# Performance work log

Measured on AMD Instinct MI355X. Metric: run time of the kernel, lower is better.

The kernel has to match this reference:

```python
import jax, jax.numpy as jnp
import numpy as np

IOU_THRESH = 0.5
NEG_POS_RATIO = 3
VAR0, VAR1 = 0.1, 0.2  # BoxCoder variances


def box_iou(a, b):
    # a: [G,4] xyxy, b: [P,4] xyxy -> [G,P]
    lt = jnp.maximum(a[:, None, :2], b[None, :, :2])
    rb = jnp.minimum(a[:, None, 2:], b[None, :, 2:])
    wh = jnp.clip(rb - lt, 0.0)
    inter = wh[..., 0] * wh[..., 1]
    area_a = (a[:, 2] - a[:, 0]) * (a[:, 3] - a[:, 1])
    area_b = (b[:, 2] - b[:, 0]) * (b[:, 3] - b[:, 1])
    return inter / (area_a[:, None] + area_b[None, :] - inter)


def xywha_to_xyxy(p):
    c, wh = p[:, :2], p[:, 2:]
    return jnp.concatenate([c - wh * 0.5, c + wh * 0.5], axis=-1)


def assign_targets(gt_boxes, gt_labels, priors_xyxy):
    # gt_boxes [G,4], gt_labels [G], priors_xyxy [P,4]
    iou = box_iou(gt_boxes, priors_xyxy)            # [G,P]
    matched_vals = iou.max(axis=0)                  # [P]
    matches = iou.argmax(axis=0)                    # [P]
    best_prior = iou.argmax(axis=1)                 # [G] best prior per target
    G = gt_boxes.shape[0]
    matches = matches.at[best_prior].set(jnp.arange(G))
    matched_vals = matched_vals.at[best_prior].set(2.0)
    labels = jnp.where(matched_vals < IOU_THRESH, 0, gt_labels[matches])  # [P]
    boxes = gt_boxes[matches]                       # [P,4]
    return boxes, labels


def encode(boxes_xyxy, priors_xywha):
    # SSD center-form encoding with variances
    ctr = (boxes_xyxy[:, :2] + boxes_xyxy[:, 2:]) * 0.5
    wh = boxes_xyxy[:, 2:] - boxes_xyxy[:, :2]
    g_c = (ctr - priors_xywha[:, :2]) / (VAR0 * priors_xywha[:, 2:])
    g_wh = jnp.log(wh / priors_xywha[:, 2:]) / VAR1
    return jnp.concatenate([g_c, g_wh], axis=-1)


def hard_negative_mask(bg_loss, labels):
    # bg_loss [B,P]: -log_softmax(logits)[...,0]; keep all positives and
    # top-(ratio*num_pos) hardest negatives per image.
    pos = labels > 0
    num_neg = pos.sum(axis=1, keepdims=True) * NEG_POS_RATIO
    loss = jnp.where(pos, -jnp.inf, bg_loss)
    order = jnp.argsort(-loss, axis=1)
    rank = jnp.argsort(order, axis=1)
    return pos | (rank < num_neg)


def reference(priors, class_logits, box_regression, gt_boxes, gt_labels):
    priors_xyxy = xywha_to_xyxy(priors)
    boxes, labels = jax.vmap(assign_targets, in_axes=(0, 0, None))(
        gt_boxes, gt_labels, priors_xyxy)            # [B,P,4], [B,P]
    regression_targets = jax.vmap(encode, in_axes=(0, None))(boxes, priors)

    logp = jax.nn.log_softmax(class_logits, axis=-1)  # [B,P,C]
    bg_loss = jax.lax.stop_gradient(-logp[..., 0])
    mask = hard_negative_mask(bg_loss, labels)        # [B,P] bool

    # masked cross-entropy, reduction='sum'
    ce = -jnp.take_along_axis(logp, labels[..., None], axis=-1)[..., 0]
    loss_classifier = jnp.sum(jnp.where(mask, ce, 0.0))

    # masked smooth-L1 (beta=1), reduction='sum' over positives
    pos = labels > 0
    d = jnp.abs(box_regression - regression_targets)
    sl1 = jnp.where(d < 1.0, 0.5 * d * d, d - 0.5)
    loss_box_reg = jnp.sum(jnp.where(pos[..., None], sl1, 0.0))

    num_pos = jnp.sum(pos).astype(class_logits.dtype)
    return loss_box_reg / num_pos, loss_classifier / num_pos


def setup_inputs() -> dict:
    key = jax.random.key(0)
    ks = jax.random.split(key, 8)
    B, P, C, G = 64, 8732, 81, 16
    # priors: xywha in [0,1] with small positive wh
    p_c = jax.random.uniform(ks[0], (P, 2), jnp.float32, 0.05, 0.95)
    p_wh = jax.random.uniform(ks[1], (P, 2), jnp.float32, 0.02, 0.25)
    priors = jnp.concatenate([p_c, p_wh], axis=-1)
    class_logits = jax.random.normal(ks[2], (B, P, C), jnp.float32)
    box_regression = jax.random.normal(ks[3], (B, P, 4), jnp.float32)
    # gt boxes: valid xyxy in [0,1] with positive size
    g_c = jax.random.uniform(ks[4], (B, G, 2), jnp.float32, 0.2, 0.8)
    g_wh = jax.random.uniform(ks[5], (B, G, 2), jnp.float32, 0.05, 0.3)
    gt_boxes = jnp.concatenate([g_c - g_wh * 0.5, g_c + g_wh * 0.5], axis=-1)
    gt_labels = jax.random.randint(ks[6], (B, G), 1, C, jnp.int32)
    return {"priors": priors, "class_logits": class_logits,
            "box_regression": box_regression, "gt_boxes": gt_boxes,
            "gt_labels": gt_labels}
```

## Files before the change

### kernel.cpp

```cpp
#include <hip/hip_runtime.h>
#include <cfloat>

#define GT 16
#define NCLS 81
#define TPB 256
#define BPT 1024
#define MAXP 8732
#define TROWS 64
#define WF4 324
#define TF4 (TROWS*NCLS/4)

__device__ __forceinline__ float smoothl1(float d){
  float a = fabsf(d);
  return a < 1.0f ? 0.5f*a*a : a - 0.5f;
}

__global__ __launch_bounds__(BPT) void bestprior(
    const float* __restrict__ priors,
    const float* __restrict__ gt_boxes,
    int*   __restrict__ best,
    float* __restrict__ ce_pos, float* __restrict__ sl1_sum,
    int* __restrict__ num_pos, float* __restrict__ out, int P)
{
  const int b = blockIdx.x;
  const int tid = threadIdx.x, wave = tid >> 6, lane = tid & 63;
  __shared__ float gx0[GT], gy0[GT], gx1[GT], gy1[GT], ga[GT];
  __shared__ float redv[16*GT]; __shared__ int redi[16*GT];
  if (tid == 0){ ce_pos[b] = 0.0f; sl1_sum[b] = 0.0f; num_pos[b] = 0; }
  if (b == 0 && tid < 2) out[tid] = 0.0f;
  if (tid < GT){
    const float4 gb = ((const float4*)gt_boxes)[b*GT + tid];
    gx0[tid]=gb.x; gy0[tid]=gb.y; gx1[tid]=gb.z; gy1[tid]=gb.w;
    ga[tid] = (gb.z-gb.x)*(gb.w-gb.y);
  }
  __syncthreads();
  float bv[GT]; int bi[GT];
  #pragma unroll
  for (int g=0; g<GT; ++g){ bv[g] = -1.0f; bi[g] = 0x7fffffff; }
  for (int p = tid; p < P; p += BPT){
    const float4 pr = ((const float4*)priors)[p];
    const float px0 = pr.x - pr.z*0.5f, py0 = pr.y - pr.w*0.5f;
    const float px1 = pr.x + pr.z*0.5f, py1 = pr.y + pr.w*0.5f;
    const float pa = (px1-px0)*(py1-py0);
    #pragma unroll
    for (int g=0; g<GT; ++g){
      const float w = fmaxf(fminf(gx1[g],px1) - fmaxf(gx0[g],px0), 0.0f);
      const float h = fmaxf(fminf(gy1[g],py1) - fmaxf(gy0[g],py0), 0.0f);
      const float inter = w*h;
      const float iou = inter / (ga[g] + pa - inter);
      if (iou > bv[g]){ bv[g] = iou; bi[g] = p; }
    }
  }
  #pragma unroll
  for (int g=0; g<GT; ++g){
    float v = bv[g]; int i = bi[g];
    for (int off=32; off>0; off>>=1){
      const float ov = __shfl_down(v, off);
      const int   oi = __shfl_down(i, off);
      if (ov > v || (ov == v && oi < i)){ v = ov; i = oi; }
    }
    if (lane == 0){ redv[wave*GT+g] = v; redi[wave*GT+g] = i; }
  }
  __syncthreads();
  if (tid < GT){
    float v = redv[tid]; int i = redi[tid];
    for (int w=1; w<16; ++w){
      const float ov = redv[w*GT+tid]; const int oi = redi[w*GT+tid];
      if (ov > v || (ov == v && oi < i)){ v = ov; i = oi; }
    }
    best[b*GT + tid] = i;
  }
}

__global__ __launch_bounds__(TPB) void fused_lse(
    const float* __restrict__ priors,
    const float* __restrict__ gt_boxes,
    const int*   __restrict__ gt_labels,
    const float* __restrict__ box_reg,
    const int*   __restrict__ best,
    const float* __restrict__ logits,
    float* __restrict__ bg,
    float* __restrict__ ce_pos,
    float* __restrict__ sl1_sum,
    int*   __restrict__ num_pos,
    int P, int NT)
{
  __shared__ float s[TROWS*NCLS];
  const int tid = threadIdx.x;
  const int wave = tid >> 6, lane = tid & 63;
  const int rl = lane >> 2, q = lane & 3;
  const int c0 = q ? (1+20*q) : 0;
  const int c1 = 21 + 20*q;
  const int G = gridDim.x;
  int t = blockIdx.x;
  if (t >= NT) return;

  float4 r0,r1,r2,r3,r4,r5;
  {
    const float4* src = (const float4*)logits + (long long)t*TF4 + wave*WF4;
    r0 = src[lane]; r1 = src[lane+64]; r2 = src[lane+128];
    r3 = src[lane+192]; r4 = src[lane+256];
    if (lane < 4) r5 = src[lane+320];
  }
  float4* sd = (float4*)(s) + wave*WF4;
  const float* x = s + wave*(WF4*4) + rl*NCLS;
  for (; t < NT; t += G){
    sd[lane] = r0; sd[lane+64] = r1; sd[lane+128] = r2;
    sd[lane+192] = r3; sd[lane+256] = r4;
    if (lane < 4) sd[lane+320] = r5;
    const int tn = t + G;
    if (tn < NT){
      const float4* src = (const float4*)logits + (long long)tn*TF4 + wave*WF4;
      r0 = src[lane]; r1 = src[lane+64]; r2 = src[lane+128];
      r3 = src[lane+192]; r4 = src[lane+256];
      if (lane < 4) r5 = src[lane+320];
    }

    const int row = t*TROWS + wave*16 + rl;
    const int b = row / P;
    const int p = row - b*P;
    int lab = 0;
    if (q == 0){
      const float4 pr = ((const float4*)priors)[p];
      const float px0 = pr.x - pr.z*0.5f, py0 = pr.y - pr.w*0.5f;
      const float px1 = pr.x + pr.z*0.5f, py1 = pr.y + pr.w*0.5f;
      const float pa = (px1-px0)*(py1-py0);
      const float4* gtb4 = (const float4*)gt_boxes + b*GT;
      float mv = -1.0f; int mi = 0;
      #pragma unroll
      for (int g=0; g<GT; ++g){
        const float4 gb = gtb4[g];
        const float w = fmaxf(fminf(gb.z,px1) - fmaxf(gb.x,px0), 0.0f);
        const float h = fmaxf(fminf(gb.w,py1) - fmaxf(gb.y,py0), 0.0f);
        const float inter = w*h;
        const float garea = (gb.z-gb.x)*(gb.w-gb.y);
        const float iou = inter / (garea + pa - inter);
        if (iou > mv){ mv = iou; mi = g; }
      }
      const int* bpp = best + b*GT;
      #pragma unroll
      for (int g2=0; g2<GT; ++g2){
        if (bpp[g2] == p){ mv = 2.0f; mi = g2; }
      }
      if (mv >= 0.5f){
        lab = gt_labels[b*GT + mi];
        const float4 gb = gtb4[mi];
        const float ctrx = (gb.x+gb.z)*0.5f, ctry = (gb.y+gb.w)*0.5f;
        const float wx = gb.z-gb.x, wy = gb.w-gb.y;
        const float tx = (ctrx - pr.x) / (0.1f*pr.z);
        const float ty = (ctry - pr.y) / (0.1f*pr.w);
        const float tw = __logf(wx/pr.z) / 0.2f;
        const float th = __logf(wy/pr.w) / 0.2f;
        const float4 br = ((const float4*)box_reg)[(long long)row];
        const float s1 = smoothl1(br.x - tx) + smoothl1(br.y - ty)
                       + smoothl1(br.z - tw) + smoothl1(br.w - th);
        atomicAdd(&sl1_sum[b], s1);
        atomicAdd(&num_pos[b], 1);
      }
    }

    float sum = 0.0f;
    for (int c = c0; c < c1; ++c) sum += __expf(x[c]);
    sum += __shfl_xor(sum, 1);
    sum += __shfl_xor(sum, 2);
    if (q == 0){
      const float lse = __logf(sum);
      float bgv;
      if (lab > 0){
        atomicAdd(&ce_pos[b], lse - x[lab]);
        bgv = 0.0f;
      } else {
        bgv = fmaxf(lse - x[0], 0.0f);
      }
      bg[row] = bgv;
    }
  }
}

__global__ __launch_bounds__(TPB) void topk_kernel(
    const float* __restrict__ bg,
    const int*   __restrict__ num_pos,
    const float* __restrict__ sl1_sum,
    const float* __restrict__ ce_pos,
    float* __restrict__ out,
    int P, int B)
{
  const int b = blockIdx.x;
  const int tid = threadIdx.x;
  const int wave = tid >> 6, lane = tid & 63;
  const int rep = tid & 15;
  __shared__ float sv[MAXP];
  __shared__ unsigned cntR[16][257];
  __shared__ unsigned s_wc[4];
  __shared__ float    s_wf[4];
  __shared__ unsigned s_prefix;
  __shared__ int s_krem, s_chosen, s_newk;

  {
    const float4* srcp = (const float4*)(bg + (long long)b * P);
    float4* dst = (float4*)sv;
    for (int j = tid; j < P/4; j += TPB) dst[j] = srcp[j];
  }
  if (tid == 0){
    const int k = 3*num_pos[b];
    s_krem = k < P ? k : P-1;
    s_prefix = 0u;
  }
  __syncthreads();

  for (int level=0; level<4; ++level){
    const int shift = 24 - 8*level;
    for (int i = tid; i < 16*257; i += TPB) ((unsigned*)cntR)[i] = 0u;
    __syncthreads();
    const unsigned pref = s_prefix;
    const int k = s_krem;
    for (int j = tid; j < P/4; j += TPB){
      const float4 f4 = ((const float4*)sv)[j];
      #pragma unroll
      for (int e=0; e<4; ++e){
        const unsigned key = __float_as_uint((&f4.x)[e]);
        const bool ok = (level == 0) || ((key >> (shift+8)) == pref);
        if (ok) atomicAdd(&cntR[rep][(key >> shift) & 255u], 1u);
      }
    }
    __syncthreads();
    const int rb = 255 - tid;
    unsigned c = 0;
    #pragma unroll
    for (int r=0; r<16; ++r) c += cntR[r][rb];
    unsigned cv = c;
    #pragma unroll
    for (int off=1; off<64; off<<=1){
      const unsigned oc = __shfl_up(cv, off);
      if (lane >= off) cv += oc;
    }
    if (lane == 63) s_wc[wave] = cv;
    __syncthreads();
    unsigned addc = 0;
    for (int w=0; w<4; ++w) if (w < wave) addc += s_wc[w];
    const unsigned S = cv - c + addc;
    if ((int)S <= k && k < (int)(S + c)){
      s_chosen = rb; s_newk = k - (int)S;
    }
    __syncthreads();
    if (tid == 0){
      s_krem = s_newk;
      s_prefix = (pref << 8) | (unsigned)s_chosen;
    }
    __syncthreads();
  }
  const unsigned T = s_prefix;
  float acc = 0.0f;
  for (int j = tid; j < P/4; j += TPB){
    const float4 f4 = ((const float4*)sv)[j];
    #pragma unroll
    for (int e=0; e<4; ++e){
      const float f = (&f4.x)[e];
      if (__float_as_uint(f) > T) acc += f;
    }
  }
  for (int off=32; off>0; off>>=1) acc += __shfl_down(acc, off);
  if (lane == 0) s_wf[wave] = acc;
  __syncthreads();
  if (tid < 64){
    float n = 0.0f;
    for (int i = tid; i < B; i += 64) n += (float)num_pos[i];
    for (int off=32; off>0; off>>=1) n += __shfl_down(n, off);
    if (tid == 0){
      const float N = n;
      const float cls = s_wf[0]+s_wf[1]+s_wf[2]+s_wf[3]
                      + (float)s_krem * __uint_as_float(T);
      atomicAdd(&out[0], sl1_sum[b] / N);
      atomicAdd(&out[1], (ce_pos[b] + cls) / N);
    }
  }
}

extern "C" void kernel_launch(void* const* d_in, const int* in_sizes, int n_in,
                              void* d_out, int out_size, void* d_ws, size_t ws_size,
                              hipStream_t stream) {
  const float* priors = (const float*)d_in[0];
  const float* logits = (const float*)d_in[1];
  const float* boxreg = (const float*)d_in[2];
  const float* gtb    = (const float*)d_in[3];
  const int*   gtl    = (const int*)d_in[4];
  const int P = in_sizes[0] / 4;
  const int B = in_sizes[4] / GT;
  const long long BP = (long long)B * P;

  char* ws = (char*)d_ws;
  float* bgv  = (float*)ws;
  int*   best = (int*)(ws + BP*4);
  float* sl1_s= (float*)(ws + BP*4 + 4096);
  int*   npos = (int*)  (ws + BP*4 + 4352);
  float* cep  = (float*)(ws + BP*4 + 4608);

  bestprior<<<B, BPT, 0, stream>>>(priors, gtb, best, cep, sl1_s, npos,
                                   (float*)d_out, P);
  const int NT = (int)(BP / TROWS);
  const int G = 1792;
  fused_lse<<<G, TPB, 0, stream>>>(priors, gtb, gtl, boxreg, best, logits,
                                   bgv, cep, sl1_s, npos, P, NT);
  topk_kernel<<<B, TPB, 0, stream>>>(bgv, npos, sl1_s, cep, (float*)d_out, P, B);
}
```

Before: 367.9 us.

## Use contiguous tile ranges per block, stage GT data in LDS, prefetch priors/box_reg

Each block now handles a contiguous range of tiles instead of a grid-stride set. That range spans at most two images, so the block caches both images' GT boxes, areas, labels and best-prior indices in shared memory once. The priors and box regression loads for the next tile are prefetched in registers alongside the logits, and the positive-box atomics move next to the CE atomic. An occupancy hint of 7 is added to launch_bounds. The cost is more register pressure and the assumption that a block's range crosses no more than one image boundary.

```diff
diff --git a/kernel.cpp b/kernel.cpp
--- a/kernel.cpp
+++ b/kernel.cpp
@@ -72,7 +72,7 @@
   }
 }
 
-__global__ __launch_bounds__(TPB) void fused_lse(
+__global__ __launch_bounds__(TPB, 7) void fused_lse(
     const float* __restrict__ priors,
     const float* __restrict__ gt_boxes,
     const int*   __restrict__ gt_labels,
@@ -86,76 +86,96 @@
     int P, int NT)
 {
   __shared__ float s[TROWS*NCLS];
+  __shared__ float sgx0[2][GT], sgy0[2][GT], sgx1[2][GT], sgy1[2][GT], sga[2][GT];
+  __shared__ int   slab[2][GT], sbp[2][GT];
   const int tid = threadIdx.x;
   const int wave = tid >> 6, lane = tid & 63;
   const int rl = lane >> 2, q = lane & 3;
   const int c0 = q ? (1+20*q) : 0;
   const int c1 = 21 + 20*q;
   const int G = gridDim.x;
-  int t = blockIdx.x;
-  if (t >= NT) return;
-
-  float4 r0,r1,r2,r3,r4,r5;
-  {
-    const float4* src = (const float4*)logits + (long long)t*TF4 + wave*WF4;
+
+  const int qn = NT / G, rn = NT % G;
+  const int k = blockIdx.x;
+  const int t0  = k < rn ? k*(qn+1) : rn*(qn+1) + (k-rn)*qn;
+  const int cnt = k < rn ? qn+1 : qn;
+  if (cnt <= 0) return;
+  const int tend = t0 + cnt;
+  const int b0 = (t0*TROWS)/P;
+  const int b1 = (tend*TROWS - 1)/P;
+  const int boundary = b1*P;
+
+  if (tid < 2*GT){
+    const int slot = tid >> 4, g = tid & 15;
+    const int bb = slot ? b1 : b0;
+    const float4 gb = ((const float4*)gt_boxes)[bb*GT + g];
+    sgx0[slot][g]=gb.x; sgy0[slot][g]=gb.y; sgx1[slot][g]=gb.z; sgy1[slot][g]=gb.w;
+    sga[slot][g] = (gb.z-gb.x)*(gb.w-gb.y);
+    slab[slot][g] = gt_labels[bb*GT + g];
+    sbp[slot][g]  = best[bb*GT + g];
+  }
+  __syncthreads();
+
+  float4 r0,r1,r2,r3,r4,r5, prn, brn;
+  auto load_logits = [&](int tt){
+    const float4* src = (const float4*)logits + (long long)tt*TF4 + wave*WF4;
     r0 = src[lane]; r1 = src[lane+64]; r2 = src[lane+128];
     r3 = src[lane+192]; r4 = src[lane+256];
     if (lane < 4) r5 = src[lane+320];
-  }
+  };
+  auto load_row = [&](int tt){
+    if (q == 0){
+      const int rw = tt*TROWS + wave*16 + rl;
+      const int bb = (rw >= boundary) ? b1 : b0;
+      prn = ((const float4*)priors)[rw - bb*P];
+      brn = ((const float4*)box_reg)[rw];
+    }
+  };
+  load_logits(t0); load_row(t0);
+
   float4* sd = (float4*)(s) + wave*WF4;
   const float* x = s + wave*(WF4*4) + rl*NCLS;
-  for (; t < NT; t += G){
+  for (int t = t0; t < tend; ++t){
     sd[lane] = r0; sd[lane+64] = r1; sd[lane+128] = r2;
     sd[lane+192] = r3; sd[lane+256] = r4;
     if (lane < 4) sd[lane+320] = r5;
-    const int tn = t + G;
-    if (tn < NT){
-      const float4* src = (const float4*)logits + (long long)tn*TF4 + wave*WF4;
-      r0 = src[lane]; r1 = src[lane+64]; r2 = src[lane+128];
-      r3 = src[lane+192]; r4 = src[lane+256];
-      if (lane < 4) r5 = src[lane+320];
-    }
-
+    const float4 pr = prn, br = brn;
     const int row = t*TROWS + wave*16 + rl;
-    const int b = row / P;
+    const int slot = (row >= boundary);
+    const int b = slot ? b1 : b0;
     const int p = row - b*P;
-    int lab = 0;
+    if (t+1 < tend){ load_logits(t+1); load_row(t+1); }
+
+    int lab = 0; float s1 = 0.0f;
     if (q == 0){
-      const float4 pr = ((const float4*)priors)[p];
       const float px0 = pr.x - pr.z*0.5f, py0 = pr.y - pr.w*0.5f;
       const float px1 = pr.x + pr.z*0.5f, py1 = pr.y + pr.w*0.5f;
       const float pa = (px1-px0)*(py1-py0);
-      const float4* gtb4 = (const float4*)gt_boxes + b*GT;
       float mv = -1.0f; int mi = 0;
       #pragma unroll
       for (int g=0; g<GT; ++g){
-        const float4 gb = gtb4[g];
-        const float w = fmaxf(fminf(gb.z,px1) - fmaxf(gb.x,px0), 0.0f);
-        const float h = fmaxf(fminf(gb.w,py1) - fmaxf(gb.y,py0), 0.0f);
+        const float w = fmaxf(fminf(sgx1[slot][g],px1) - fmaxf(sgx0[slot][g],px0), 0.0f);
+        const float h = fmaxf(fminf(sgy1[slot][g],py1) - fmaxf(sgy0[slot][g],py0), 0.0f);
         const float inter = w*h;
-        const float garea = (gb.z-gb.x)*(gb.w-gb.y);
-        const float iou = inter / (garea + pa - inter);
+        const float iou = inter / (sga[slot][g] + pa - inter);
         if (iou > mv){ mv = iou; mi = g; }
       }
-      const int* bpp = best + b*GT;
       #pragma unroll
       for (int g2=0; g2<GT; ++g2){
-        if (bpp[g2] == p){ mv = 2.0f; mi = g2; }
+        if (sbp[slot][g2] == p){ mv = 2.0f; mi = g2; }
       }
       if (mv >= 0.5f){
-        lab = gt_labels[b*GT + mi];
-        const float4 gb = gtb4[mi];
-        const float ctrx = (gb.x+gb.z)*0.5f, ctry = (gb.y+gb.w)*0.5f;
-        const float wx = gb.z-gb.x, wy = gb.w-gb.y;
+        lab = slab[slot][mi];
+        const float gbx0 = sgx0[slot][mi], gby0 = sgy0[slot][mi];
+        const float gbx1 = sgx1[slot][mi], gby1 = sgy1[slot][mi];
+        const float ctrx = (gbx0+gbx1)*0.5f, ctry = (gby0+gby1)*0.5f;
+        const float wx = gbx1-gbx0, wy = gby1-gby0;
         const float tx = (ctrx - pr.x) / (0.1f*pr.z);
         const float ty = (ctry - pr.y) / (0.1f*pr.w);
         const float tw = __logf(wx/pr.z) / 0.2f;
         const float th = __logf(wy/pr.w) / 0.2f;
-        const float4 br = ((const float4*)box_reg)[(long long)row];
-        const float s1 = smoothl1(br.x - tx) + smoothl1(br.y - ty)
-                       + smoothl1(br.z - tw) + smoothl1(br.w - th);
-        atomicAdd(&sl1_sum[b], s1);
-        atomicAdd(&num_pos[b], 1);
+        s1 = smoothl1(br.x - tx) + smoothl1(br.y - ty)
+           + smoothl1(br.z - tw) + smoothl1(br.w - th);
       }
     }
 
@@ -168,6 +188,8 @@
       float bgv;
       if (lab > 0){
         atomicAdd(&ce_pos[b], lse - x[lab]);
+        atomicAdd(&sl1_sum[b], s1);
+        atomicAdd(&num_pos[b], 1);
         bgv = 0.0f;
       } else {
         bgv = fmaxf(lse - x[0], 0.0f);
```

New measurement: 517.1 us. +40.6%, slower.
